# Performance work log

Measured on AMD Instinct MI355X. Metric: run time of the kernel, lower is better.

The kernel has to match this reference:

```python
import jax, jax.numpy as jnp
import numpy as np

B, T, I, H = 64, 1024, 1024, 1024


def setup_inputs() -> dict:
    key = jax.random.key(0)
    k1, k2, k3, k4, k5 = jax.random.split(key, 5)
    s_i = 1.0 / np.sqrt(I)
    s_h = 1.0 / np.sqrt(H)
    return {
        "input": jax.random.normal(k1, (B, T, I), dtype=jnp.float32),
        "hidden": jnp.zeros((B, H), dtype=jnp.float32),
        "W_ih": jax.random.uniform(k2, (H, I), jnp.float32, -s_i, s_i),
        "b_ih": jax.random.uniform(k3, (H,), jnp.float32, -s_i, s_i),
        "W_hh": jax.random.uniform(k4, (H, H), jnp.float32, -s_h, s_h),
        "b_hh": jax.random.uniform(k5, (H,), jnp.float32, -s_h, s_h),
    }


def reference(input, hidden, W_ih, b_ih, W_hh, b_hh):
    # Precompute the input projection for all timesteps in one big GEMM:
    # x_proj[b, t, h] = input @ W_ih^T + b_ih  (same math as per-step Linear)
    x_proj = jnp.einsum("bti,hi->bth", input, W_ih) + b_ih + b_hh

    def step(h, xp_t):
        h_new = jnp.tanh(xp_t + h @ W_hh.T)
        return h_new, h_new

    # scan over time: xp has shape (T, B, H)
    h_last, outs = jax.lax.scan(step, hidden, jnp.swapaxes(x_proj, 0, 1))
    output = jnp.swapaxes(outs, 0, 1)  # (B, T, H)
    return output, h_last
```

## Files before the change

### kernel.cpp

```cpp
#include <hip/hip_runtime.h>
#include <hip/hip_bf16.h>

#define TDIM 1024
#define HDIM 1024
#define IDIM 1024
#define BSZ  64

typedef __attribute__((ext_vector_type(4))) float  floatx4;
typedef __attribute__((ext_vector_type(2))) float  floatx2;
typedef __attribute__((ext_vector_type(8))) short  shortx8;

static __device__ __forceinline__ short f2bf(float x) {
    unsigned u = __builtin_bit_cast(unsigned, x);
    u += 0x7fffu + ((u >> 16) & 1u);
    return (short)(u >> 16);
}

static __device__ __forceinline__ shortx8 pack8(floatx4 a, floatx4 b) {
    shortx8 r;
    r[0] = f2bf(a[0]); r[1] = f2bf(a[1]); r[2] = f2bf(a[2]); r[3] = f2bf(a[3]);
    r[4] = f2bf(b[0]); r[5] = f2bf(b[1]); r[6] = f2bf(b[2]); r[7] = f2bf(b[3]);
    return r;
}

static __device__ __forceinline__ unsigned long long ld_mall8(const unsigned* p) {
    unsigned long long v;
    asm volatile("global_load_dwordx2 %0, %1, off sc0 sc1"
                 : "=v"(v) : "v"(p) : "memory");
    return v;
}
static __device__ __forceinline__ void st_tag(unsigned* p, unsigned v) {
    asm volatile("global_store_dword %0, %1, off sc0 sc1" :: "v"(p), "v"(v) : "memory");
}

__global__ __launch_bounds__(256, 2)
void xp_gemm(const float* __restrict__ A, const float* __restrict__ W,
             const float* __restrict__ bih, const float* __restrict__ bhh,
             float* __restrict__ out)
{
    __shared__ short As[128 * 72];
    __shared__ short Bs[128 * 72];

    const int tid  = threadIdx.x;
    const int bx   = blockIdx.x;
    const int m0   = (bx >> 3) * 128;
    const int n0   = (bx & 7) * 128;
    const int lane = tid & 63;
    const int w    = tid >> 6;
    const int wm   = w & 1, wn = w >> 1;
    const int col  = lane & 15, quad = lane >> 4;

    const int srow = tid >> 1;
    const int scol = (tid & 1) * 32;
    const float* ap = A + (size_t)(m0 + srow) * IDIM + scol;
    const float* wp = W + (size_t)(n0 + srow) * IDIM + scol;
    short* asw = As + srow * 72 + scol;
    short* bsw = Bs + srow * 72 + scol;

    floatx4 acc[4][4];
#pragma unroll
    for (int i = 0; i < 4; i++)
#pragma unroll
        for (int j = 0; j < 4; j++) acc[i][j] = (floatx4){0.f, 0.f, 0.f, 0.f};

    for (int kt = 0; kt < IDIM; kt += 64) {
        floatx4 av[8], bv[8];
        const floatx4* pa = (const floatx4*)(ap + kt);
        const floatx4* pb = (const floatx4*)(wp + kt);
#pragma unroll
        for (int q = 0; q < 8; q++) { av[q] = pa[q]; bv[q] = pb[q]; }
        __syncthreads();
#pragma unroll
        for (int q = 0; q < 4; q++) {
            *(shortx8*)(asw + q * 8) = pack8(av[2 * q], av[2 * q + 1]);
            *(shortx8*)(bsw + q * 8) = pack8(bv[2 * q], bv[2 * q + 1]);
        }
        __syncthreads();
#pragma unroll
        for (int kb = 0; kb < 64; kb += 32) {
            shortx8 af[4], bf[4];
#pragma unroll
            for (int i = 0; i < 4; i++)
                af[i] = *(const shortx8*)(As + (wm * 64 + i * 16 + col) * 72 + kb + quad * 8);
#pragma unroll
            for (int j = 0; j < 4; j++)
                bf[j] = *(const shortx8*)(Bs + (wn * 64 + j * 16 + col) * 72 + kb + quad * 8);
#pragma unroll
            for (int i = 0; i < 4; i++)
#pragma unroll
                for (int j = 0; j < 4; j++)
                    acc[i][j] = __builtin_amdgcn_mfma_f32_16x16x32_bf16(af[i], bf[j], acc[i][j], 0, 0, 0);
        }
    }

#pragma unroll
    for (int j = 0; j < 4; j++) {
        const int n = n0 + wn * 64 + j * 16 + col;
        const float bias = bih[n] + bhh[n];
#pragma unroll
        for (int i = 0; i < 4; i++) {
            const int mb = m0 + wm * 64 + i * 16 + quad * 4;
#pragma unroll
            for (int r = 0; r < 4; r++)
                out[(size_t)(mb + r) * HDIM + n] = acc[i][j][r] + bias;
        }
    }
}

__global__ __launch_bounds__(512, 1)
void rnn_rec(float* __restrict__ out,
             const float* __restrict__ Whh, const float* __restrict__ h0,
             unsigned* __restrict__ hexch)
{
    __shared__ short hlds[16 * 1032];

    const int tid  = threadIdx.x;
    const int g    = blockIdx.x >> 3;
    const int role = blockIdx.x & 7;
    const int lane = tid & 63;
    const int w    = tid >> 6;
    const int col  = lane & 15, quad = lane >> 4;
    const int nglob = role * 128 + w * 16 + col;
    const int b0   = quad * 4;

    {
        unsigned* z = (unsigned*)(hlds + 8 * 1032);
        for (int i = tid; i < 4 * 1032; i += 512) z[i] = 0u;
    }

    shortx8 bfrag[32];
    {
        const float* wrow = Whh + (size_t)nglob * HDIM + quad * 8;
#pragma unroll
        for (int kb = 0; kb < 32; kb++) {
            const floatx4* p = (const floatx4*)(wrow + kb * 32);
            bfrag[kb] = pack8(p[0], p[1]);
        }
    }
    __syncthreads();

    const int bsafe = b0 & 7;
    float xp[4], xpn[4];
#pragma unroll
    for (int r = 0; r < 4; r++)
        xp[r] = __builtin_nontemporal_load(
            out + (size_t)(g * 8 + bsafe + r) * (TDIM * HDIM) + nglob);

    const int cc = w * 128 + lane * 2;
    const unsigned gbase = (unsigned)(g * 8192 + cc);

    for (int t = 0; t < TDIM; ++t) {
        if (t == 0) {
            const int c2 = tid * 2;
#pragma unroll
            for (int j = 0; j < 8; j++) {
                floatx2 f = *(const floatx2*)(h0 + (size_t)(g * 8 + j) * HDIM + c2);
                const unsigned pk = (unsigned)(unsigned short)f2bf(f[0]) |
                                    ((unsigned)(unsigned short)f2bf(f[1]) << 16);
                *(unsigned*)(hlds + j * 1032 + c2) = pk;
            }
        } else {
            const unsigned long long msk = 0x0000FFFF0000FFFFULL;
            const unsigned long long tt  = (unsigned long long)(unsigned)t;
            const unsigned long long pat = tt | (tt << 32);
            const unsigned* base = hexch + ((unsigned)(t & 1) << 16) + gbase;
            unsigned long long hv[8];
            int guard = 0;
            for (;;) {
#pragma unroll
                for (int j = 0; j < 8; j++)
                    hv[j] = ld_mall8(base + (size_t)j * 1024);
                asm volatile("s_waitcnt vmcnt(0)" ::: "memory");
                __builtin_amdgcn_sched_barrier(0);
                bool bad = false;
#pragma unroll
                for (int j = 0; j < 8; j++)
                    bad |= ((hv[j] & msk) != pat);
                if (!__any((int)bad)) break;
                if (++guard > (1 << 16)) break;
                asm volatile("s_sleep 1");
            }
#pragma unroll
            for (int j = 0; j < 8; j++) {
                const unsigned pk = (unsigned)((hv[j] >> 16) & 0xFFFFu) |
                                    (unsigned)((hv[j] >> 32) & 0xFFFF0000u);
                *(unsigned*)(hlds + j * 1032 + cc) = pk;
            }
        }

        if (t + 1 < TDIM) {
#pragma unroll
            for (int r = 0; r < 4; r++)
                xpn[r] = __builtin_nontemporal_load(
                    out + (size_t)(g * 8 + bsafe + r) * (TDIM * HDIM) + (size_t)(t + 1) * HDIM + nglob);
        }

        asm volatile("s_waitcnt lgkmcnt(0)" ::: "memory");
        __builtin_amdgcn_s_barrier();

        floatx4 a0 = (floatx4){0.f, 0.f, 0.f, 0.f};
        floatx4 a1 = a0, a2 = a0, a3 = a0;
#pragma unroll
        for (int kb = 0; kb < 32; kb += 4) {
            shortx8 f0 = *(const shortx8*)(hlds + col * 1032 + (kb + 0) * 32 + quad * 8);
            shortx8 f1 = *(const shortx8*)(hlds + col * 1032 + (kb + 1) * 32 + quad * 8);
            shortx8 f2 = *(const shortx8*)(hlds + col * 1032 + (kb + 2) * 32 + quad * 8);
            shortx8 f3 = *(const shortx8*)(hlds + col * 1032 + (kb + 3) * 32 + quad * 8);
            a0 = __builtin_amdgcn_mfma_f32_16x16x32_bf16(f0, bfrag[kb + 0], a0, 0, 0, 0);
            a1 = __builtin_amdgcn_mfma_f32_16x16x32_bf16(f1, bfrag[kb + 1], a1, 0, 0, 0);
            a2 = __builtin_amdgcn_mfma_f32_16x16x32_bf16(f2, bfrag[kb + 2], a2, 0, 0, 0);
            a3 = __builtin_amdgcn_mfma_f32_16x16x32_bf16(f3, bfrag[kb + 3], a3, 0, 0, 0);
        }
        floatx4 acc = (a0 + a1) + (a2 + a3);

        float hval[4];
#pragma unroll
        for (int r = 0; r < 4; r++)
            hval[r] = tanhf(xp[r] + acc[r]);

        if (t + 1 < TDIM) {
            unsigned* hd = hexch + ((unsigned)((t + 1) & 1) << 16) + (unsigned)(g * 8192);
            const unsigned tag = (unsigned)(t + 1);
            if (b0 < 8) {
#pragma unroll
                for (int r = 0; r < 4; r++)
                    st_tag(hd + (size_t)(b0 + r) * 1024 + nglob,
                           ((unsigned)(unsigned short)f2bf(hval[r]) << 16) | tag);
            }
        }

        if (b0 < 8) {
#pragma unroll
            for (int r = 0; r < 4; r++) {
                const int b = g * 8 + b0 + r;
                const size_t oidx = (size_t)b * (TDIM * HDIM) + (size_t)t * HDIM + nglob;
                out[oidx] = hval[r];
                if (t == TDIM - 1)
                    out[(size_t)BSZ * TDIM * HDIM + (size_t)b * HDIM + nglob] = hval[r];
            }
        }
#pragma unroll
        for (int r = 0; r < 4; r++) xp[r] = xpn[r];

        if (t + 1 < TDIM) {
            asm volatile("s_waitcnt lgkmcnt(0)" ::: "memory");
            __builtin_amdgcn_s_barrier();
        }
    }
}

extern "C" void kernel_launch(void* const* d_in, const int* in_sizes, int n_in,
                              void* d_out, int out_size, void* d_ws, size_t ws_size,
                              hipStream_t stream)
{
    const float* input = (const float*)d_in[0];
    const float* h0    = (const float*)d_in[1];
    const float* W_ih  = (const float*)d_in[2];
    const float* b_ih  = (const float*)d_in[3];
    const float* W_hh  = (const float*)d_in[4];
    const float* b_hh  = (const float*)d_in[5];
    float* out = (float*)d_out;

    unsigned* hexch = (unsigned*)d_ws;

    hipMemsetAsync(hexch, 0, (size_t)2 * 65536 * 4, stream);

    xp_gemm<<<dim3(4096), dim3(256), 0, stream>>>(input, W_ih, b_ih, b_hh, out);
    rnn_rec<<<dim3(64),   dim3(512), 0, stream>>>(out, W_hh, h0, hexch);
}
```

Before: 3.865 ms.

## Interleave two batch groups per block to hide cross-block exchange latency

Each workgroup now handles two 8-batch groups, A and B, in alternating phases. While it computes the MFMA recurrence step for one group, it issues the loads that poll the other group's exchanged hidden state, so the exchange latency overlaps with compute. The LDS layout changes from padded rows to an XOR-swizzled layout to avoid bank conflicts, and the grid is halved to 32 blocks. The trade-off is half the CUs doing the serial work and a tighter sequence of hand-placed vmcnt waits, which is fragile if the compiler reorders loads.

```diff
diff --git a/kernel.cpp b/kernel.cpp
--- a/kernel.cpp
+++ b/kernel.cpp
@@ -32,6 +32,8 @@
 static __device__ __forceinline__ void st_tag(unsigned* p, unsigned v) {
     asm volatile("global_store_dword %0, %1, off sc0 sc1" :: "v"(p), "v"(v) : "memory");
 }
+
+#define SWZ(row, bytecol) ((((row) * 2048) + (bytecol)) ^ (((row) & 7) << 4))
 
 __global__ __launch_bounds__(256, 2)
 void xp_gemm(const float* __restrict__ A, const float* __restrict__ W,
@@ -107,25 +109,149 @@
     }
 }
 
+static __device__ __forceinline__ void phase(
+    const short* ldsX, short* ldsY, const shortx8* bfrag, float* xp,
+    float* __restrict__ out, unsigned* __restrict__ hexch,
+    int t, int ts, int batX, int grpX, int grpY,
+    int nglob, int b0, int bsafe, int col, int quad, int w, int lane)
+{
+    floatx4 a0 = (floatx4){0.f, 0.f, 0.f, 0.f};
+    floatx4 a1 = a0, a2 = a0, a3 = a0;
+    const char* lb = (const char*)ldsX;
+    const int rb = col * 2048;
+    const int sx = (col & 7) << 4;
+
+#pragma unroll
+    for (int kb = 0; kb < 16; kb += 4) {
+        shortx8 f0 = *(const shortx8*)(lb + ((rb + (kb + 0) * 64 + quad * 16) ^ sx));
+        shortx8 f1 = *(const shortx8*)(lb + ((rb + (kb + 1) * 64 + quad * 16) ^ sx));
+        shortx8 f2 = *(const shortx8*)(lb + ((rb + (kb + 2) * 64 + quad * 16) ^ sx));
+        shortx8 f3 = *(const shortx8*)(lb + ((rb + (kb + 3) * 64 + quad * 16) ^ sx));
+        a0 = __builtin_amdgcn_mfma_f32_16x16x32_bf16(f0, bfrag[kb + 0], a0, 0, 0, 0);
+        a1 = __builtin_amdgcn_mfma_f32_16x16x32_bf16(f1, bfrag[kb + 1], a1, 0, 0, 0);
+        a2 = __builtin_amdgcn_mfma_f32_16x16x32_bf16(f2, bfrag[kb + 2], a2, 0, 0, 0);
+        a3 = __builtin_amdgcn_mfma_f32_16x16x32_bf16(f3, bfrag[kb + 3], a3, 0, 0, 0);
+    }
+
+    unsigned long long hv[8];
+    const unsigned* psrc = hexch;
+    if (ts >= 0) {
+        psrc = hexch + ((unsigned)(ts & 1) << 16) + grpY * 8192 + (w * 128 + lane * 2);
+        __builtin_amdgcn_sched_barrier(0);
+#pragma unroll
+        for (int j = 0; j < 8; j++) hv[j] = ld_mall8(psrc + (size_t)j * 1024);
+        __builtin_amdgcn_sched_barrier(0);
+    }
+
+#pragma unroll
+    for (int kb = 16; kb < 32; kb += 4) {
+        shortx8 f0 = *(const shortx8*)(lb + ((rb + (kb + 0) * 64 + quad * 16) ^ sx));
+        shortx8 f1 = *(const shortx8*)(lb + ((rb + (kb + 1) * 64 + quad * 16) ^ sx));
+        shortx8 f2 = *(const shortx8*)(lb + ((rb + (kb + 2) * 64 + quad * 16) ^ sx));
+        shortx8 f3 = *(const shortx8*)(lb + ((rb + (kb + 3) * 64 + quad * 16) ^ sx));
+        a0 = __builtin_amdgcn_mfma_f32_16x16x32_bf16(f0, bfrag[kb + 0], a0, 0, 0, 0);
+        a1 = __builtin_amdgcn_mfma_f32_16x16x32_bf16(f1, bfrag[kb + 1], a1, 0, 0, 0);
+        a2 = __builtin_amdgcn_mfma_f32_16x16x32_bf16(f2, bfrag[kb + 2], a2, 0, 0, 0);
+        a3 = __builtin_amdgcn_mfma_f32_16x16x32_bf16(f3, bfrag[kb + 3], a3, 0, 0, 0);
+    }
+    floatx4 acc = (a0 + a1) + (a2 + a3);
+
+    if (ts >= 0)
+        asm volatile("s_waitcnt vmcnt(20)"
+                     : "+v"(xp[0]), "+v"(xp[1]), "+v"(xp[2]), "+v"(xp[3]) :: "memory");
+    else
+        asm volatile("s_waitcnt vmcnt(0)"
+                     : "+v"(xp[0]), "+v"(xp[1]), "+v"(xp[2]), "+v"(xp[3]) :: "memory");
+    __builtin_amdgcn_sched_barrier(0);
+
+    float hval[4];
+#pragma unroll
+    for (int r = 0; r < 4; r++) hval[r] = tanhf(xp[r] + acc[r]);
+
+    if (t + 1 < TDIM && b0 < 8) {
+        unsigned* hd = hexch + ((unsigned)((t + 1) & 1) << 16) + grpX * 8192;
+        const unsigned tag = (unsigned)(t + 1);
+#pragma unroll
+        for (int r = 0; r < 4; r++)
+            st_tag(hd + (size_t)(b0 + r) * 1024 + nglob,
+                   ((unsigned)(unsigned short)f2bf(hval[r]) << 16) | tag);
+    }
+    if (b0 < 8) {
+#pragma unroll
+        for (int r = 0; r < 4; r++) {
+            const int b = batX + b0 + r;
+            out[(size_t)b * (TDIM * HDIM) + (size_t)t * HDIM + nglob] = hval[r];
+            if (t == TDIM - 1)
+                out[(size_t)BSZ * TDIM * HDIM + (size_t)b * HDIM + nglob] = hval[r];
+        }
+    }
+    if (t + 1 < TDIM) {
+#pragma unroll
+        for (int r = 0; r < 4; r++) {
+            const float* pf = out + (size_t)(batX + bsafe + r) * (TDIM * HDIM)
+                                  + (size_t)(t + 1) * HDIM + nglob;
+            asm volatile("global_load_dword %0, %1, off" : "=v"(xp[r]) : "v"(pf));
+        }
+    }
+
+    if (ts >= 0) {
+        asm volatile("s_waitcnt vmcnt(12)"
+                     : "+v"(hv[0]), "+v"(hv[1]), "+v"(hv[2]), "+v"(hv[3]),
+                       "+v"(hv[4]), "+v"(hv[5]), "+v"(hv[6]), "+v"(hv[7]) :: "memory");
+        __builtin_amdgcn_sched_barrier(0);
+        const unsigned long long msk = 0x0000FFFF0000FFFFULL;
+        const unsigned long long tt  = (unsigned long long)(unsigned)ts;
+        const unsigned long long pat = tt | (tt << 32);
+        bool bad = false;
+#pragma unroll
+        for (int j = 0; j < 8; j++) bad |= ((hv[j] & msk) != pat);
+        int guard = 0;
+        while (__any((int)bad)) {
+            if (++guard > (1 << 13)) break;
+            asm volatile("s_sleep 1");
+#pragma unroll
+            for (int j = 0; j < 8; j++) hv[j] = ld_mall8(psrc + (size_t)j * 1024);
+            asm volatile("s_waitcnt vmcnt(0)" ::: "memory");
+            __builtin_amdgcn_sched_barrier(0);
+            bad = false;
+#pragma unroll
+            for (int j = 0; j < 8; j++) bad |= ((hv[j] & msk) != pat);
+        }
+        const int ccb = (w * 128 + lane * 2) * 2;
+#pragma unroll
+        for (int j = 0; j < 8; j++) {
+            const unsigned pk = (unsigned)((hv[j] >> 16) & 0xFFFFu) |
+                                (unsigned)((hv[j] >> 32) & 0xFFFF0000u);
+            *(unsigned*)((char*)ldsY + SWZ(j, ccb)) = pk;
+        }
+    }
+    asm volatile("s_waitcnt lgkmcnt(0)" ::: "memory");
+    __builtin_amdgcn_s_barrier();
+}
+
 __global__ __launch_bounds__(512, 1)
 void rnn_rec(float* __restrict__ out,
              const float* __restrict__ Whh, const float* __restrict__ h0,
              unsigned* __restrict__ hexch)
 {
-    __shared__ short hlds[16 * 1032];
+    __shared__ short lds[2][16 * 1024];
 
     const int tid  = threadIdx.x;
-    const int g    = blockIdx.x >> 3;
+    const int pair = blockIdx.x >> 3;
     const int role = blockIdx.x & 7;
     const int lane = tid & 63;
     const int w    = tid >> 6;
     const int col  = lane & 15, quad = lane >> 4;
     const int nglob = role * 128 + w * 16 + col;
     const int b0   = quad * 4;
+    const int bsafe = b0 & 7;
+    const int batA = pair * 16, batB = pair * 16 + 8;
+    const int grpA = pair * 2, grpB = pair * 2 + 1;
 
     {
-        unsigned* z = (unsigned*)(hlds + 8 * 1032);
-        for (int i = tid; i < 4 * 1032; i += 512) z[i] = 0u;
+        unsigned* z0 = (unsigned*)(lds[0] + 8 * 1024);
+        unsigned* z1 = (unsigned*)(lds[1] + 8 * 1024);
+        for (int i = tid; i < 4096; i += 512) { z0[i] = 0u; z1[i] = 0u; }
     }
 
     shortx8 bfrag[32];
@@ -137,115 +263,36 @@
             bfrag[kb] = pack8(p[0], p[1]);
         }
     }
+
+    {
+        const int cb = tid * 4;
+#pragma unroll
+        for (int j = 0; j < 8; j++) {
+            floatx2 fA = *(const floatx2*)(h0 + (size_t)(batA + j) * HDIM + tid * 2);
+            floatx2 fB = *(const floatx2*)(h0 + (size_t)(batB + j) * HDIM + tid * 2);
+            const unsigned pA = (unsigned)(unsigned short)f2bf(fA[0]) |
+                                ((unsigned)(unsigned short)f2bf(fA[1]) << 16);
+            const unsigned pB = (unsigned)(unsigned short)f2bf(fB[0]) |
+                                ((unsigned)(unsigned short)f2bf(fB[1]) << 16);
+            *(unsigned*)((char*)lds[0] + SWZ(j, cb)) = pA;
+            *(unsigned*)((char*)lds[1] + SWZ(j, cb)) = pB;
+        }
+    }
+    float xpA[4], xpB[4];
+#pragma unroll
+    for (int r = 0; r < 4; r++) {
+        xpA[r] = out[(size_t)(batA + bsafe + r) * (TDIM * HDIM) + nglob];
+        xpB[r] = out[(size_t)(batB + bsafe + r) * (TDIM * HDIM) + nglob];
+    }
     __syncthreads();
 
-    const int bsafe = b0 & 7;
-    float xp[4], xpn[4];
-#pragma unroll
-    for (int r = 0; r < 4; r++)
-        xp[r] = __builtin_nontemporal_load(
-            out + (size_t)(g * 8 + bsafe + r) * (TDIM * HDIM) + nglob);
-
-    const int cc = w * 128 + lane * 2;
-    const unsigned gbase = (unsigned)(g * 8192 + cc);
-
     for (int t = 0; t < TDIM; ++t) {
-        if (t == 0) {
-            const int c2 = tid * 2;
-#pragma unroll
-            for (int j = 0; j < 8; j++) {
-                floatx2 f = *(const floatx2*)(h0 + (size_t)(g * 8 + j) * HDIM + c2);
-                const unsigned pk = (unsigned)(unsigned short)f2bf(f[0]) |
-                                    ((unsigned)(unsigned short)f2bf(f[1]) << 16);
-                *(unsigned*)(hlds + j * 1032 + c2) = pk;
-            }
-        } else {
-            const unsigned long long msk = 0x0000FFFF0000FFFFULL;
-            const unsigned long long tt  = (unsigned long long)(unsigned)t;
-            const unsigned long long pat = tt | (tt << 32);
-            const unsigned* base = hexch + ((unsigned)(t & 1) << 16) + gbase;
-            unsigned long long hv[8];
-            int guard = 0;
-            for (;;) {
-#pragma unroll
-                for (int j = 0; j < 8; j++)
-                    hv[j] = ld_mall8(base + (size_t)j * 1024);
-                asm volatile("s_waitcnt vmcnt(0)" ::: "memory");
-                __builtin_amdgcn_sched_barrier(0);
-                bool bad = false;
-#pragma unroll
-                for (int j = 0; j < 8; j++)
-                    bad |= ((hv[j] & msk) != pat);
-                if (!__any((int)bad)) break;
-                if (++guard > (1 << 16)) break;
-                asm volatile("s_sleep 1");
-            }
-#pragma unroll
-            for (int j = 0; j < 8; j++) {
-                const unsigned pk = (unsigned)((hv[j] >> 16) & 0xFFFFu) |
-                                    (unsigned)((hv[j] >> 32) & 0xFFFF0000u);
-                *(unsigned*)(hlds + j * 1032 + cc) = pk;
-            }
-        }
-
-        if (t + 1 < TDIM) {
-#pragma unroll
-            for (int r = 0; r < 4; r++)
-                xpn[r] = __builtin_nontemporal_load(
-                    out + (size_t)(g * 8 + bsafe + r) * (TDIM * HDIM) + (size_t)(t + 1) * HDIM + nglob);
-        }
-
-        asm volatile("s_waitcnt lgkmcnt(0)" ::: "memory");
-        __builtin_amdgcn_s_barrier();
-
-        floatx4 a0 = (floatx4){0.f, 0.f, 0.f, 0.f};
-        floatx4 a1 = a0, a2 = a0, a3 = a0;
-#pragma unroll
-        for (int kb = 0; kb < 32; kb += 4) {
-            shortx8 f0 = *(const shortx8*)(hlds + col * 1032 + (kb + 0) * 32 + quad * 8);
-            shortx8 f1 = *(const shortx8*)(hlds + col * 1032 + (kb + 1) * 32 + quad * 8);
-            shortx8 f2 = *(const shortx8*)(hlds + col * 1032 + (kb + 2) * 32 + quad * 8);
-            shortx8 f3 = *(const shortx8*)(hlds + col * 1032 + (kb + 3) * 32 + quad * 8);
-            a0 = __builtin_amdgcn_mfma_f32_16x16x32_bf16(f0, bfrag[kb + 0], a0, 0, 0, 0);
-            a1 = __builtin_amdgcn_mfma_f32_16x16x32_bf16(f1, bfrag[kb + 1], a1, 0, 0, 0);
-            a2 = __builtin_amdgcn_mfma_f32_16x16x32_bf16(f2, bfrag[kb + 2], a2, 0, 0, 0);
-            a3 = __builtin_amdgcn_mfma_f32_16x16x32_bf16(f3, bfrag[kb + 3], a3, 0, 0, 0);
-        }
-        floatx4 acc = (a0 + a1) + (a2 + a3);
-
-        float hval[4];
-#pragma unroll
-        for (int r = 0; r < 4; r++)
-            hval[r] = tanhf(xp[r] + acc[r]);
-
-        if (t + 1 < TDIM) {
-            unsigned* hd = hexch + ((unsigned)((t + 1) & 1) << 16) + (unsigned)(g * 8192);
-            const unsigned tag = (unsigned)(t + 1);
-            if (b0 < 8) {
-#pragma unroll
-                for (int r = 0; r < 4; r++)
-                    st_tag(hd + (size_t)(b0 + r) * 1024 + nglob,
-                           ((unsigned)(unsigned short)f2bf(hval[r]) << 16) | tag);
-            }
-        }
-
-        if (b0 < 8) {
-#pragma unroll
-            for (int r = 0; r < 4; r++) {
-                const int b = g * 8 + b0 + r;
-                const size_t oidx = (size_t)b * (TDIM * HDIM) + (size_t)t * HDIM + nglob;
-                out[oidx] = hval[r];
-                if (t == TDIM - 1)
-                    out[(size_t)BSZ * TDIM * HDIM + (size_t)b * HDIM + nglob] = hval[r];
-            }
-        }
-#pragma unroll
-        for (int r = 0; r < 4; r++) xp[r] = xpn[r];
-
-        if (t + 1 < TDIM) {
-            asm volatile("s_waitcnt lgkmcnt(0)" ::: "memory");
-            __builtin_amdgcn_s_barrier();
-        }
+        phase(lds[0], lds[1], bfrag, xpA, out, hexch,
+              t, (t == 0) ? -1 : t, batA, grpA, grpB,
+              nglob, b0, bsafe, col, quad, w, lane);
+        phase(lds[1], lds[0], bfrag, xpB, out, hexch,
+              t, (t + 1 < TDIM) ? (t + 1) : -1, batB, grpB, grpA,
+              nglob, b0, bsafe, col, quad, w, lane);
     }
 }
 
@@ -266,5 +313,5 @@
     hipMemsetAsync(hexch, 0, (size_t)2 * 65536 * 4, stream);
 
     xp_gemm<<<dim3(4096), dim3(256), 0, stream>>>(input, W_ih, b_ih, b_hh, out);
-    rnn_rec<<<dim3(64),   dim3(512), 0, stream>>>(out, W_hh, h0, hexch);
-}
+    rnn_rec<<<dim3(32),   dim3(512), 0, stream>>>(out, W_hh, h0, hexch);
+}
```

Measured after the change: 7.433 ms. +92.3%, slower.
